# Optimization experiments

Hardware: AMD Instinct MI355X
Metric: run time of the kernel (lower is better)

## Reference

```python
import jax, jax.numpy as jnp
import numpy as np

B, S, T = 128, 1024, 512
VOCAB, E, HE, HD, ATT = 1000, 128, 64, 66, 32


def setup_inputs() -> dict:
    key = jax.random.key(0)
    ks = jax.random.split(key, 14)
    p = lambda k, shape: (jax.random.normal(k, shape, dtype=jnp.float32) * 0.05)
    return {
        'x': jax.random.randint(ks[0], (B, S), 0, VOCAB, dtype=jnp.int32),
        'c': jax.random.normal(ks[1], (B, T), dtype=jnp.float32),
        'emb': p(ks[2], (VOCAB, E)),
        'enc_Wih': p(ks[3], (4 * HE, E)),
        'enc_Whh': p(ks[4], (4 * HE, HE)),
        'enc_b': p(ks[5], (4 * HE,)),
        'att_fc_W': p(ks[6], (HE, E)),
        'att_fc_b': p(ks[7], (HE,)),
        'att_w_W': p(ks[8], (ATT, HE)),
        'att_w_b': p(ks[9], (ATT,)),
        'dec_Wih': p(ks[10], (4 * HD, ATT)),
        'dec_Whh': p(ks[11], (4 * HD, HD)),
        'dec_b': p(ks[12], (4 * HD,)),
        'fin_W': p(ks[13], (E, HD)),
        'fin_b': jnp.zeros((E,), dtype=jnp.float32),
    }


def _lstm_seq(xs, W_ih, W_hh, b, H):
    # xs: [B, S, in]; PyTorch gate order i, f, g, o
    bsz = xs.shape[0]
    gx = jnp.einsum('bsi,gi->bsg', xs, W_ih) + b  # [B,S,4H]

    def step(carry, g_t):
        h, c = carry
        g = g_t + h @ W_hh.T
        i, f, gg, o = jnp.split(g, 4, axis=-1)
        c = jax.nn.sigmoid(f) * c + jax.nn.sigmoid(i) * jnp.tanh(gg)
        h = jax.nn.sigmoid(o) * jnp.tanh(c)
        return (h, c), h

    h0 = jnp.zeros((bsz, H), xs.dtype)
    (_, _), hs = jax.lax.scan(step, (h0, h0), jnp.swapaxes(gx, 0, 1))
    return jnp.swapaxes(hs, 0, 1)  # [B,S,H]


def reference(x, c, emb, enc_Wih, enc_Whh, enc_b, att_fc_W, att_fc_b,
              att_w_W, att_w_b, dec_Wih, dec_Whh, dec_b, fin_W, fin_b):
    # encoder: embed + LSTM, returns full sequence of hidden states [B,S,64]
    enc = _lstm_seq(emb[x], enc_Wih, enc_Whh, enc_b, HE)
    bsz, steps = x.shape[0], c.shape[1]
    # initial decoder input: embedding of token 0, broadcast over batch
    x0 = jnp.broadcast_to(emb[0], (bsz, E))
    h0 = jnp.zeros((bsz, HD), enc.dtype)

    def step(carry, _):
        xemb, h, cc = carry
        # attend(a=xemb, A=enc)
        a = xemb @ att_fc_W.T + att_fc_b                     # [B,64]
        A = a[:, None, :] * enc                              # [B,S,64]
        alpha = jax.nn.softmax(
            jnp.tanh(jnp.einsum('bse,ae->bsa', A, att_w_W) + att_w_b),
            axis=-1)                                         # [B,S,32]
        beta = alpha.sum(axis=1)                             # [B,32]
        # decoder LSTM cell (one timestep)
        g = beta @ dec_Wih.T + h @ dec_Whh.T + dec_b
        i, f, gg, o = jnp.split(g, 4, axis=-1)
        cc = jax.nn.sigmoid(f) * cc + jax.nn.sigmoid(i) * jnp.tanh(gg)
        h = jax.nn.sigmoid(o) * jnp.tanh(cc)
        xemb = h @ fin_W.T + fin_b                           # feed back via final_fc
        return (xemb, h, cc), h

    _, hs = jax.lax.scan(step, (x0, h0, h0), None, length=steps)
    return jnp.swapaxes(hs, 0, 1)  # [B,T,66]
```

## Files before the change

### kernel.cpp

```cpp
#include <hip/hip_runtime.h>
#include <hip/hip_bf16.h>

#define kB 128
#define kS 1024
#define kT 512
#define kV 1000
#define kE 128
#define kHE 64
#define kHD 66
#define kATT 32
#define kGE 256
#define kGD 264

typedef __attribute__((ext_vector_type(4))) float f32x4;
typedef __attribute__((ext_vector_type(8))) short bf16x8;
typedef __attribute__((ext_vector_type(8))) unsigned short u16x8;

__device__ __forceinline__ unsigned short f2bf(float f) {
  unsigned int u = __builtin_bit_cast(unsigned int, f);
  u += 0x7FFFu + ((u >> 16) & 1u);
  return (unsigned short)(u >> 16);
}
__device__ __forceinline__ float rcp_(float x) { return __builtin_amdgcn_rcpf(x); }
__device__ __forceinline__ float fsig(float x)  { return rcp_(1.0f + __expf(-x)); }
__device__ __forceinline__ float ftanh(float x) { return 1.0f - 2.0f * rcp_(1.0f + __expf(2.0f * x)); }
__device__ __forceinline__ float fexp2(float z) {
#if __has_builtin(__builtin_amdgcn_exp2f)
  return __builtin_amdgcn_exp2f(z);
#else
  return __expf(z * 0.6931471805599453f);
#endif
}
__device__ __forceinline__ const unsigned short* launder_us(const unsigned short* p) {
  asm volatile("" : "+s"(p));
  return p;
}
__device__ __forceinline__ float dpp_red16(float v) {
  int x = __builtin_bit_cast(int, v);
  v += __builtin_bit_cast(float, __builtin_amdgcn_update_dpp(0, x, 0xB1, 0xf, 0xf, true));
  x = __builtin_bit_cast(int, v);
  v += __builtin_bit_cast(float, __builtin_amdgcn_update_dpp(0, x, 0x4E, 0xf, 0xf, true));
  x = __builtin_bit_cast(int, v);
  v += __builtin_bit_cast(float, __builtin_amdgcn_update_dpp(0, x, 0x124, 0xf, 0xf, true));
  x = __builtin_bit_cast(int, v);
  v += __builtin_bit_cast(float, __builtin_amdgcn_update_dpp(0, x, 0x128, 0xf, 0xf, true));
  return v;
}
#define DPPB(v, ctrl) __builtin_bit_cast(float, __builtin_amdgcn_update_dpp(0, __builtin_bit_cast(int, (v)), (ctrl), 0xf, 0xf, true))

__global__ __launch_bounds__(256) void prep_kernel(
    const float* __restrict__ emb, const float* __restrict__ enc_Wih,
    const float* __restrict__ enc_b, const float* __restrict__ enc_Whh,
    const float* __restrict__ att_fc_W, const float* __restrict__ att_fc_b,
    const float* __restrict__ att_w_W,
    const float* __restrict__ fin_W, const float* __restrict__ fin_b,
    const float* __restrict__ dec_Wih, const float* __restrict__ dec_Whh,
    const float* __restrict__ dec_b,
    float* __restrict__ embW, unsigned short* __restrict__ decF,
    unsigned short* __restrict__ encF, unsigned short* __restrict__ afF,
    float* __restrict__ wregF, float* __restrict__ dbias,
    float* __restrict__ wh64, float* __restrict__ wh65,
    float* __restrict__ abias, float* __restrict__ ainit) {
  int bid = blockIdx.x, tid = threadIdx.x;
  if (bid < kV) {
    float acc = enc_b[tid];
    const float* er = emb + bid * kE;
    const float* wr = enc_Wih + tid * kE;
    for (int e = 0; e < kE; ++e) acc += er[e] * wr[e];
    embW[bid * kGE + tid] = acc;
  } else if (bid == kV) {
    for (int i = tid; i < 17 * 3 * 64 * 8; i += 256) {
      int jj = i & 7, lane = (i >> 3) & 63, ts = i >> 9;
      int tile = ts / 3, ks = ts - tile * 3;
      int jp = tile * 16 + (lane & 15);
      int cell = jp >> 2, gate = jp & 3;
      int k = ks * 32 + ((lane >> 4) << 3) + jj;
      float v = 0.f;
      if (cell < kHD) {
        int j = gate * kHD + cell;
        if (k < 32) v = dec_Wih[j * kATT + k];
        else v = dec_Whh[j * kHD + (k - 32)];
      }
      decF[i] = f2bf(v);
    }
  } else if (bid == kV + 1) {
    for (int i = tid; i < 16 * 2 * 64 * 8; i += 256) {
      int jj = i & 7, lane = (i >> 3) & 63, ts = i >> 9;
      int tile = ts >> 1, ks = ts & 1;
      int j = tile * 16 + (lane & 15);
      int k = ks * 32 + ((lane >> 4) << 3) + jj;
      encF[i] = f2bf(enc_Whh[j * kHE + k]);
    }
  } else if (bid == kV + 2) {
    for (int i = tid; i < 4 * 3 * 64 * 8; i += 256) {
      int jj = i & 7, lane = (i >> 3) & 63, ts = i >> 9;
      int tile = ts / 3, ks = ts - tile * 3;
      int aidx = tile * 16 + (lane & 15);
      int m = ks * 32 + ((lane >> 4) << 3) + jj;
      float v = 0.f;
      if (m < kHD)
        for (int e = 0; e < kE; ++e) v += att_fc_W[aidx * kE + e] * fin_W[e * kHD + m];
      afF[i] = f2bf(v);
    }
  } else if (bid == kV + 3) {
    for (int i = tid; i < 8 * 64 * 4; i += 256) {
      int c = i & 3, lane = (i >> 2) & 63, jq = i >> 8;
      int half = jq & 1, kc = (jq >> 1) & 1, mt = jq >> 2;
      wregF[i] = att_w_W[(mt * 16 + (lane & 15)) * kHE + kc * 32 + ((lane >> 4) << 3) + half * 4 + c];
    }
  } else if (bid == kV + 4) {
    for (int jp = tid; jp < kGD; jp += 256) {
      int cell = jp >> 2, gate = jp & 3;
      int j = gate * kHD + cell;
      float s = 0.f;
      for (int m = 0; m < kATT; ++m) s += dec_Wih[j * kATT + m];
      dbias[jp] = dec_b[j] + 32.0f * s;
      wh64[jp] = dec_Whh[j * kHD + 64];
      wh65[jp] = dec_Whh[j * kHD + 65];
    }
  } else {
    if (tid < kHE) {
      float acc = att_fc_b[tid];
      for (int e = 0; e < kE; ++e) acc += att_fc_W[tid * kE + e] * fin_b[e];
      abias[tid] = acc;
    } else if (tid < 2 * kHE) {
      int a = tid - kHE;
      float acc = att_fc_b[a];
      for (int e = 0; e < kE; ++e) acc += emb[e] * att_fc_W[a * kE + e];
      ainit[a] = acc;
    }
  }
}

__global__ __launch_bounds__(256)
__attribute__((amdgpu_waves_per_eu(1, 1)))
void enc_kernel(
    const int* __restrict__ x, const float* __restrict__ embW,
    const unsigned short* __restrict__ encF, float* __restrict__ out) {
  __shared__ struct __align__(16) {
    unsigned short xe[64];
    float gbuf[kGE];
    int toks[kS];
  } sm;
  const int b = blockIdx.x, t = threadIdx.x, lane = t & 63, wv = t >> 6;

  for (int i = t; i < kS; i += 256) sm.toks[i] = x[b * kS + i];
  if (t < 64) sm.xe[t] = 0;

  u16x8 eQ[4][2];
  #pragma unroll
  for (int q = 0; q < 4; ++q)
    #pragma unroll
    for (int ks = 0; ks < 2; ++ks)
      eQ[q][ks] = *(const u16x8*)&encF[(((wv * 4 + q) * 2 + ks) * 64 + lane) * 8];
  __syncthreads();

  float gx0 = 0, gx1 = 0, gx2 = 0, gx3 = 0;
  if (lane < 16) {
    int tok = sm.toks[0];
    gx0 = embW[tok * kGE + wv * 64 + 0 + lane];
    gx1 = embW[tok * kGE + wv * 64 + 16 + lane];
    gx2 = embW[tok * kGE + wv * 64 + 32 + lane];
    gx3 = embW[tok * kGE + wv * 64 + 48 + lane];
  }
  float cE = 0.0f;
  unsigned short* eg = (unsigned short*)(out + (size_t)b * (kT * kHD));

  for (int s = 0; s < kS; ++s) {
    union { u16x8 u; bf16x8 v; } xa0, xa1;
    xa0.u = *(const u16x8*)&sm.xe[(lane >> 4) << 3];
    xa1.u = *(const u16x8*)&sm.xe[32 + ((lane >> 4) << 3)];
    float gn0 = 0, gn1 = 0, gn2 = 0, gn3 = 0;
    int tokn = sm.toks[(s + 1 < kS) ? (s + 1) : s];
    if (lane < 16) {
      gn0 = embW[tokn * kGE + wv * 64 + 0 + lane];
      gn1 = embW[tokn * kGE + wv * 64 + 16 + lane];
      gn2 = embW[tokn * kGE + wv * 64 + 32 + lane];
      gn3 = embW[tokn * kGE + wv * 64 + 48 + lane];
    }
    f32x4 z = {0.f, 0.f, 0.f, 0.f};
    f32x4 a0 = __builtin_amdgcn_mfma_f32_16x16x32_bf16(xa0.v, eQ[0][0], z, 0, 0, 0);
    a0 = __builtin_amdgcn_mfma_f32_16x16x32_bf16(xa1.v, eQ[0][1], a0, 0, 0, 0);
    f32x4 a1 = __builtin_amdgcn_mfma_f32_16x16x32_bf16(xa0.v, eQ[1][0], z, 0, 0, 0);
    a1 = __builtin_amdgcn_mfma_f32_16x16x32_bf16(xa1.v, eQ[1][1], a1, 0, 0, 0);
    f32x4 a2 = __builtin_amdgcn_mfma_f32_16x16x32_bf16(xa0.v, eQ[2][0], z, 0, 0, 0);
    a2 = __builtin_amdgcn_mfma_f32_16x16x32_bf16(xa1.v, eQ[2][1], a2, 0, 0, 0);
    f32x4 a3 = __builtin_amdgcn_mfma_f32_16x16x32_bf16(xa0.v, eQ[3][0], z, 0, 0, 0);
    a3 = __builtin_amdgcn_mfma_f32_16x16x32_bf16(xa1.v, eQ[3][1], a3, 0, 0, 0);
    if (lane < 16) {
      sm.gbuf[wv * 64 + 0 + lane]  = a0[0] + gx0;
      sm.gbuf[wv * 64 + 16 + lane] = a1[0] + gx1;
      sm.gbuf[wv * 64 + 32 + lane] = a2[0] + gx2;
      sm.gbuf[wv * 64 + 48 + lane] = a3[0] + gx3;
    }
    __syncthreads();
    if (t < 64) {
      float gi = sm.gbuf[t], gf = sm.gbuf[64 + t], gg = sm.gbuf[128 + t], go = sm.gbuf[192 + t];
      cE = fsig(gf) * cE + fsig(gi) * ftanh(gg);
      float h = fsig(go) * ftanh(cE);
      unsigned short hb = f2bf(h);
      sm.xe[t] = hb;
      eg[s * 64 + ((((t >> 3) ^ (s & 7)) << 3) | (t & 7))] = hb;
    }
    __syncthreads();
    gx0 = gn0; gx1 = gn1; gx2 = gn2; gx3 = gn3;
  }
}

struct __align__(16) DSm {
  unsigned short enc[kS * kHE];
  float wregL[8 * 64 * 4];
  unsigned short afL[4 * 3 * 64 * 8];
  float dbL[kGD];
  float wh64L[kGD];
  float wh65L[kGD];
  float absL[64];
  float aa[64];
  float beta[32];
  unsigned short xv[2][160];
  float hh2[2][2];
};

union U8 { u16x8 u; bf16x8 v; };

__global__ __launch_bounds__(512, 2)
void dec_kernel(
    const float* __restrict__ att_w_b,
    const unsigned short* __restrict__ decF, const unsigned short* __restrict__ afF,
    const float* __restrict__ wregF_ws, const float* __restrict__ dbias_ws,
    const float* __restrict__ wh64_ws, const float* __restrict__ wh65_ws,
    const float* __restrict__ abias_ws, const float* __restrict__ ainit_ws,
    float* __restrict__ out) {
  __shared__ DSm sm;
  const int b = blockIdx.x, t = threadIdx.x, lane = t & 63, wv = t >> 6;
  const int lr = lane & 15, g = lane >> 4;

  {
    const u16x8* src = (const u16x8*)(out + (size_t)b * (kT * kHD));
    u16x8* dst = (u16x8*)sm.enc;
    #pragma unroll
    for (int i = 0; i < 16; ++i) dst[t + i * 512] = src[t + i * 512];
  }
  ((f32x4*)sm.wregL)[t] = ((const f32x4*)wregF_ws)[t];
  for (int i = t; i < 768; i += 512) ((u16x8*)sm.afL)[i] = ((const u16x8*)afF)[i];
  for (int i = t; i < kGD; i += 512) {
    sm.dbL[i] = dbias_ws[i];
    sm.wh64L[i] = wh64_ws[i];
    sm.wh65L[i] = wh65_ws[i];
  }
  if (t < 64) { sm.absL[t] = abias_ws[t]; sm.aa[t] = ainit_ws[t]; }
  if (t < 32) sm.beta[t] = 0.f;
  for (int i = t; i < 320; i += 512) ((unsigned short*)sm.xv)[i] = 0;
  if (t < 4) ((float*)sm.hh2)[t] = 0.f;

  f32x4 wb0, wb1;
  #pragma unroll
  for (int r = 0; r < 4; ++r) {
    wb0[r] = att_w_b[g * 4 + r];
    wb1[r] = att_w_b[16 + g * 4 + r];
  }
  const int sbase = wv * 128;
  const int tileA = wv, tileB = wv + 8;
  const bool has3 = (wv == 7);

  U8 qa[3], qb[3];
  #pragma unroll
  for (int ks = 0; ks < 3; ++ks) {
    qa[ks].u = *(const u16x8*)&decF[((tileA * 3 + ks) * 64 + lane) * 8];
    qb[ks].u = *(const u16x8*)&decF[((tileB * 3 + ks) * 64 + lane) * 8];
  }
  float cDa = 0.0f, cDb = 0.0f, cDc = 0.0f;
  __syncthreads();

  for (int step = 0; step < kT; ++step) {
    const int cb = step & 1, nb = cb ^ 1;
    U8 qc[3];
    {
      const f32x4* aap = (const f32x4*)sm.aa;
      const f32x4* wrl = (const f32x4*)sm.wregL;
      bf16x8 af[2][2];
      #pragma unroll
      for (int kc = 0; kc < 2; ++kc) {
        f32x4 a0v = aap[kc * 8 + g * 2];
        f32x4 a1v = aap[kc * 8 + g * 2 + 1];
        #pragma unroll
        for (int mt = 0; mt < 2; ++mt) {
          f32x4 w0 = wrl[((mt * 2 + kc) * 2 + 0) * 64 + lane];
          f32x4 w1 = wrl[((mt * 2 + kc) * 2 + 1) * 64 + lane];
          union { bf16x8 v; __hip_bfloat162 h2[4]; } tmp;
          tmp.h2[0] = __float22bfloat162_rn(make_float2(w0.x * a0v.x, w0.y * a0v.y));
          tmp.h2[1] = __float22bfloat162_rn(make_float2(w0.z * a0v.z, w0.w * a0v.w));
          tmp.h2[2] = __float22bfloat162_rn(make_float2(w1.x * a1v.x, w1.y * a1v.y));
          tmp.h2[3] = __float22bfloat162_rn(make_float2(w1.z * a1v.z, w1.w * a1v.w));
          af[mt][kc] = tmp.v;
        }
      }
      float betaAcc[2][4] = {};
      float amax = 0.0f;
      #pragma unroll
      for (int nt = 0; nt < 8; ++nt) {
        int s = sbase + nt * 16 + lr;
        int sw = s & 7;
        U8 e0, e1;
        e0.u = *(const u16x8*)&sm.enc[s * kHE + ((g ^ sw) << 3)];
        e1.u = *(const u16x8*)&sm.enc[s * kHE + (((4 + g) ^ sw) << 3)];
        f32x4 acc0 = __builtin_amdgcn_mfma_f32_16x16x32_bf16(af[0][0], e0.v, wb0, 0, 0, 0);
        acc0 = __builtin_amdgcn_mfma_f32_16x16x32_bf16(af[0][1], e1.v, acc0, 0, 0, 0);
        f32x4 acc1 = __builtin_amdgcn_mfma_f32_16x16x32_bf16(af[1][0], e0.v, wb1, 0, 0, 0);
        acc1 = __builtin_amdgcn_mfma_f32_16x16x32_bf16(af[1][1], e1.v, acc1, 0, 0, 0);
        float u0[4], u1[4], dsum = 0.f;
        #pragma unroll
        for (int r = 0; r < 4; ++r) {
          float x0 = acc0[r], x1 = acc1[r];
          amax = fmaxf(amax, fmaxf(__builtin_fabsf(x0), __builtin_fabsf(x1)));
          u0[r] = fexp2(x0 * __builtin_fmaf(x0 * x0, -0.48089835f, 1.44269504f));
          u1[r] = fexp2(x1 * __builtin_fmaf(x1 * x1, -0.48089835f, 1.44269504f));
          dsum += u0[r] + u1[r];
        }
        dsum += __shfl_xor(dsum, 16);
        dsum += __shfl_xor(dsum, 32);
        float invd = rcp_(dsum);
        #pragma unroll
        for (int r = 0; r < 4; ++r) {
          betaAcc[0][r] += u0[r] * invd;
          betaAcc[1][r] += u1[r] * invd;
        }
      }
      if (__builtin_expect(__any(amax > 0.35f), 0)) {
        #pragma unroll
        for (int mt = 0; mt < 2; ++mt)
          #pragma unroll
          for (int r = 0; r < 4; ++r) betaAcc[mt][r] = 0.f;
        for (int nt = 0; nt < 8; ++nt) {
          int s = sbase + nt * 16 + lr;
          int sw = s & 7;
          U8 e0, e1;
          e0.u = *(const u16x8*)&sm.enc[s * kHE + ((g ^ sw) << 3)];
          e1.u = *(const u16x8*)&sm.enc[s * kHE + (((4 + g) ^ sw) << 3)];
          f32x4 acc0 = __builtin_amdgcn_mfma_f32_16x16x32_bf16(af[0][0], e0.v, wb0, 0, 0, 0);
          acc0 = __builtin_amdgcn_mfma_f32_16x16x32_bf16(af[0][1], e1.v, acc0, 0, 0, 0);
          f32x4 acc1 = __builtin_amdgcn_mfma_f32_16x16x32_bf16(af[1][0], e0.v, wb1, 0, 0, 0);
          acc1 = __builtin_amdgcn_mfma_f32_16x16x32_bf16(af[1][1], e1.v, acc1, 0, 0, 0);
          float u0[4], u1[4], dsum = 0.f;
          for (int r = 0; r < 4; ++r) {
            u0[r] = __expf(tanhf(acc0[r]));
            u1[r] = __expf(tanhf(acc1[r]));
            dsum += u0[r] + u1[r];
          }
          dsum += __shfl_xor(dsum, 16);
          dsum += __shfl_xor(dsum, 32);
          float invd = rcp_(dsum);
          for (int r = 0; r < 4; ++r) {
            betaAcc[0][r] += u0[r] * invd;
            betaAcc[1][r] += u1[r] * invd;
          }
        }
      }
      if (has3) {
        const unsigned short* dFp = launder_us(decF);
        #pragma unroll
        for (int ks = 0; ks < 3; ++ks)
          qc[ks].u = *(const u16x8*)&dFp[((16 * 3 + ks) * 64 + lane) * 8];
      }
      #pragma unroll
      for (int mt = 0; mt < 2; ++mt)
        #pragma unroll
        for (int r = 0; r < 4; ++r) {
          float v = dpp_red16(betaAcc[mt][r]);
          if (lr == 0) atomicAdd(&sm.beta[mt * 16 + g * 4 + r], v);
        }
    }
    __syncthreads();
    {
      const f32x4* pb = (const f32x4*)sm.beta;
      f32x4 b0 = pb[g * 2], b1 = pb[g * 2 + 1];
      union { bf16x8 v; __hip_bfloat162 h2[4]; } bfr;
      bfr.h2[0] = __float22bfloat162_rn(make_float2(b0.x - 32.f, b0.y - 32.f));
      bfr.h2[1] = __float22bfloat162_rn(make_float2(b0.z - 32.f, b0.w - 32.f));
      bfr.h2[2] = __float22bfloat162_rn(make_float2(b1.x - 32.f, b1.y - 32.f));
      bfr.h2[3] = __float22bfloat162_rn(make_float2(b1.z - 32.f, b1.w - 32.f));
      U8 xg1, xg2;
      xg1.u = *(const u16x8*)&sm.xv[cb][32 + (g << 3)];
      xg2.u = *(const u16x8*)&sm.xv[cb][64 + (g << 3)];
      float hh0 = sm.hh2[cb][0], hh1 = sm.hh2[cb][1];
      float* op = out + ((size_t)b * kT + step) * kHD;
      const int gate = lane & 3;
      const float kk = (gate == 2) ? 2.0f : 1.0f;
      f32x4 z = {0.f, 0.f, 0.f, 0.f};
      {
        f32x4 ga = __builtin_amdgcn_mfma_f32_16x16x32_bf16(bfr.v, qa[0].v, z, 0, 0, 0);
        ga = __builtin_amdgcn_mfma_f32_16x16x32_bf16(xg1.v, qa[1].v, ga, 0, 0, 0);
        ga = __builtin_amdgcn_mfma_f32_16x16x32_bf16(xg2.v, qa[2].v, ga, 0, 0, 0);
        int jp = tileA * 16 + lr;
        float xg = ga[0] + sm.dbL[jp] + sm.wh64L[jp] * hh0 + sm.wh65L[jp] * hh1;
        float y = fsig(kk * xg);
        float v = (gate == 2) ? (2.0f * y - 1.0f) : y;
        float q0 = DPPB(v, 0x00), q1 = DPPB(v, 0x55), q2 = DPPB(v, 0xAA), q3 = DPPB(v, 0xFF);
        float cn = q1 * cDa + q0 * q2;
        cDa = cn;
        float h = q3 * ftanh(cn);
        if (gate == 0 && lane < 16) {
          int cell = jp >> 2;
          sm.xv[nb][32 + cell] = f2bf(h);
          op[cell] = h;
        }
      }
      {
        f32x4 gb = __builtin_amdgcn_mfma_f32_16x16x32_bf16(bfr.v, qb[0].v, z, 0, 0, 0);
        gb = __builtin_amdgcn_mfma_f32_16x16x32_bf16(xg1.v, qb[1].v, gb, 0, 0, 0);
        gb = __builtin_amdgcn_mfma_f32_16x16x32_bf16(xg2.v, qb[2].v, gb, 0, 0, 0);
        int jp = tileB * 16 + lr;
        float xg = gb[0] + sm.dbL[jp] + sm.wh64L[jp] * hh0 + sm.wh65L[jp] * hh1;
        float y = fsig(kk * xg);
        float v = (gate == 2) ? (2.0f * y - 1.0f) : y;
        float q0 = DPPB(v, 0x00), q1 = DPPB(v, 0x55), q2 = DPPB(v, 0xAA), q3 = DPPB(v, 0xFF);
        float cn = q1 * cDb + q0 * q2;
        cDb = cn;
        float h = q3 * ftanh(cn);
        if (gate == 0 && lane < 16) {
          int cell = jp >> 2;
          sm.xv[nb][32 + cell] = f2bf(h);
          op[cell] = h;
        }
      }
      if (has3) {
        f32x4 gc = __builtin_amdgcn_mfma_f32_16x16x32_bf16(bfr.v, qc[0].v, z, 0, 0, 0);
        gc = __builtin_amdgcn_mfma_f32_16x16x32_bf16(xg1.v, qc[1].v, gc, 0, 0, 0);
        gc = __builtin_amdgcn_mfma_f32_16x16x32_bf16(xg2.v, qc[2].v, gc, 0, 0, 0);
        int jp = 256 + (lane & 7);
        float xg = gc[0] + sm.dbL[jp] + sm.wh64L[jp] * hh0 + sm.wh65L[jp] * hh1;
        float y = fsig(kk * xg);
        float v = (gate == 2) ? (2.0f * y - 1.0f) : y;
        float q0 = DPPB(v, 0x00), q1 = DPPB(v, 0x55), q2 = DPPB(v, 0xAA), q3 = DPPB(v, 0xFF);
        float cn = q1 * cDc + q0 * q2;
        cDc = cn;
        float h = q3 * ftanh(cn);
        if (gate == 0 && lane < 8) {
          int cell = 64 + (lane >> 2);
          sm.xv[nb][32 + cell] = f2bf(h);
          sm.hh2[nb][lane >> 2] = h;
          op[cell] = h;
        }
      }
    }
    __syncthreads();
    if (wv == 0) {
      U8 y0, y1, y2;
      y0.u = *(const u16x8*)&sm.xv[nb][32 + (g << 3)];
      y1.u = *(const u16x8*)&sm.xv[nb][64 + (g << 3)];
      y2.u = *(const u16x8*)&sm.xv[nb][96 + (g << 3)];
      f32x4 z = {0.f, 0.f, 0.f, 0.f};
      #pragma unroll
      for (int tt = 0; tt < 4; ++tt) {
        U8 f0, f1, f2;
        f0.u = *(const u16x8*)&sm.afL[((tt * 3 + 0) * 64 + lane) * 8];
        f1.u = *(const u16x8*)&sm.afL[((tt * 3 + 1) * 64 + lane) * 8];
        f2.u = *(const u16x8*)&sm.afL[((tt * 3 + 2) * 64 + lane) * 8];
        f32x4 acc = __builtin_amdgcn_mfma_f32_16x16x32_bf16(y0.v, f0.v, z, 0, 0, 0);
        acc = __builtin_amdgcn_mfma_f32_16x16x32_bf16(y1.v, f1.v, acc, 0, 0, 0);
        acc = __builtin_amdgcn_mfma_f32_16x16x32_bf16(y2.v, f2.v, acc, 0, 0, 0);
        if (lane < 16) sm.aa[tt * 16 + lane] = acc[0] + sm.absL[tt * 16 + lane];
      }
      if (lane < 32) sm.beta[lane] = 0.f;
    }
    __syncthreads();
  }
}

extern "C" void kernel_launch(void* const* d_in, const int* in_sizes, int n_in,
                              void* d_out, int out_size, void* d_ws, size_t ws_size,
                              hipStream_t stream) {
  const int*   x        = (const int*)d_in[0];
  const float* emb      = (const float*)d_in[2];
  const float* enc_Wih  = (const float*)d_in[3];
  const float* enc_Whh  = (const float*)d_in[4];
  const float* enc_b    = (const float*)d_in[5];
  const float* att_fc_W = (const float*)d_in[6];
  const float* att_fc_b = (const float*)d_in[7];
  const float* att_w_W  = (const float*)d_in[8];
  const float* att_w_b  = (const float*)d_in[9];
  const float* dec_Wih  = (const float*)d_in[10];
  const float* dec_Whh  = (const float*)d_in[11];
  const float* dec_b    = (const float*)d_in[12];
  const float* fin_W    = (const float*)d_in[13];
  const float* fin_b    = (const float*)d_in[14];
  float* out = (float*)d_out;

  float* embW = (float*)d_ws;
  unsigned short* decF = (unsigned short*)(embW + kV * kGE);
  unsigned short* encF = decF + 17 * 3 * 64 * 8;
  unsigned short* afF  = encF + 16 * 2 * 64 * 8;
  float* wregF = (float*)(afF + 4 * 3 * 64 * 8);
  float* dbias = wregF + 8 * 64 * 4;
  float* wh64  = dbias + kGD;
  float* wh65  = wh64 + kGD;
  float* abias = wh65 + kGD;
  float* ainit = abias + kHE;

  prep_kernel<<<dim3(kV + 6), dim3(256), 0, stream>>>(
      emb, enc_Wih, enc_b, enc_Whh, att_fc_W, att_fc_b, att_w_W, fin_W, fin_b,
      dec_Wih, dec_Whh, dec_b, embW, decF, encF, afF, wregF, dbias, wh64, wh65,
      abias, ainit);
  enc_kernel<<<dim3(kB), dim3(256), 0, stream>>>(x, embW, encF, out);
  dec_kernel<<<dim3(kB), dim3(512), 0, stream>>>(
      att_w_b, decF, afF, wregF, dbias, wh64, wh65, abias, ainit, out);
}
```

Before: 2.823 ms.

## Interleave encoder LSTM gates per cell and fuse cell update into MFMA waves

Reorders the encoder gate weights and the precomputed embedding-gate table so the four gates of each cell sit in adjacent lanes. Each wave then computes the cell update in registers with DPP broadcasts, and tanh is expressed through a scaled sigmoid. The hidden-state buffer is double-buffered, which removes the shared gate buffer and one of the two barriers per timestep on the serial critical path. The cost is redundant activation math across lanes and reliance on the DPPB macro for lane shuffles.

```diff
diff --git a/kernel.cpp b/kernel.cpp
--- a/kernel.cpp
+++ b/kernel.cpp
@@ -67,7 +67,7 @@
     const float* er = emb + bid * kE;
     const float* wr = enc_Wih + tid * kE;
     for (int e = 0; e < kE; ++e) acc += er[e] * wr[e];
-    embW[bid * kGE + tid] = acc;
+    embW[bid * kGE + (tid & 63) * 4 + (tid >> 6)] = acc;
   } else if (bid == kV) {
     for (int i = tid; i < 17 * 3 * 64 * 8; i += 256) {
       int jj = i & 7, lane = (i >> 3) & 63, ts = i >> 9;
@@ -87,7 +87,9 @@
     for (int i = tid; i < 16 * 2 * 64 * 8; i += 256) {
       int jj = i & 7, lane = (i >> 3) & 63, ts = i >> 9;
       int tile = ts >> 1, ks = ts & 1;
-      int j = tile * 16 + (lane & 15);
+      int jp = tile * 16 + (lane & 15);
+      int cell = jp >> 2, gate = jp & 3;
+      int j = gate * kHE + cell;
       int k = ks * 32 + ((lane >> 4) << 3) + jj;
       encF[i] = f2bf(enc_Whh[j * kHE + k]);
     }
@@ -138,14 +140,16 @@
     const int* __restrict__ x, const float* __restrict__ embW,
     const unsigned short* __restrict__ encF, float* __restrict__ out) {
   __shared__ struct __align__(16) {
-    unsigned short xe[64];
-    float gbuf[kGE];
+    unsigned short xe[2][64];
     int toks[kS];
   } sm;
   const int b = blockIdx.x, t = threadIdx.x, lane = t & 63, wv = t >> 6;
+  const int lr = lane & 15;
+  const int gate = lane & 3;
+  const float kk = (gate == 2) ? 2.0f : 1.0f;
 
   for (int i = t; i < kS; i += 256) sm.toks[i] = x[b * kS + i];
-  if (t < 64) sm.xe[t] = 0;
+  if (t < 128) ((unsigned short*)sm.xe)[t] = 0;
 
   u16x8 eQ[4][2];
   #pragma unroll
@@ -155,55 +159,47 @@
       eQ[q][ks] = *(const u16x8*)&encF[(((wv * 4 + q) * 2 + ks) * 64 + lane) * 8];
   __syncthreads();
 
-  float gx0 = 0, gx1 = 0, gx2 = 0, gx3 = 0;
-  if (lane < 16) {
+  float gxq[4];
+  {
     int tok = sm.toks[0];
-    gx0 = embW[tok * kGE + wv * 64 + 0 + lane];
-    gx1 = embW[tok * kGE + wv * 64 + 16 + lane];
-    gx2 = embW[tok * kGE + wv * 64 + 32 + lane];
-    gx3 = embW[tok * kGE + wv * 64 + 48 + lane];
-  }
-  float cE = 0.0f;
+    #pragma unroll
+    for (int q = 0; q < 4; ++q) gxq[q] = embW[tok * kGE + wv * 64 + q * 16 + lr];
+  }
+  float cEq[4] = {0.f, 0.f, 0.f, 0.f};
   unsigned short* eg = (unsigned short*)(out + (size_t)b * (kT * kHD));
 
   for (int s = 0; s < kS; ++s) {
+    const int cb = s & 1, nb = cb ^ 1;
     union { u16x8 u; bf16x8 v; } xa0, xa1;
-    xa0.u = *(const u16x8*)&sm.xe[(lane >> 4) << 3];
-    xa1.u = *(const u16x8*)&sm.xe[32 + ((lane >> 4) << 3)];
-    float gn0 = 0, gn1 = 0, gn2 = 0, gn3 = 0;
+    xa0.u = *(const u16x8*)&sm.xe[cb][(lane >> 4) << 3];
+    xa1.u = *(const u16x8*)&sm.xe[cb][32 + ((lane >> 4) << 3)];
+    float gn[4];
     int tokn = sm.toks[(s + 1 < kS) ? (s + 1) : s];
-    if (lane < 16) {
-      gn0 = embW[tokn * kGE + wv * 64 + 0 + lane];
-      gn1 = embW[tokn * kGE + wv * 64 + 16 + lane];
-      gn2 = embW[tokn * kGE + wv * 64 + 32 + lane];
-      gn3 = embW[tokn * kGE + wv * 64 + 48 + lane];
-    }
+    #pragma unroll
+    for (int q = 0; q < 4; ++q) gn[q] = embW[tokn * kGE + wv * 64 + q * 16 + lr];
+
     f32x4 z = {0.f, 0.f, 0.f, 0.f};
-    f32x4 a0 = __builtin_amdgcn_mfma_f32_16x16x32_bf16(xa0.v, eQ[0][0], z, 0, 0, 0);
-    a0 = __builtin_amdgcn_mfma_f32_16x16x32_bf16(xa1.v, eQ[0][1], a0, 0, 0, 0);
-    f32x4 a1 = __builtin_amdgcn_mfma_f32_16x16x32_bf16(xa0.v, eQ[1][0], z, 0, 0, 0);
-    a1 = __builtin_amdgcn_mfma_f32_16x16x32_bf16(xa1.v, eQ[1][1], a1, 0, 0, 0);
-    f32x4 a2 = __builtin_amdgcn_mfma_f32_16x16x32_bf16(xa0.v, eQ[2][0], z, 0, 0, 0);
-    a2 = __builtin_amdgcn_mfma_f32_16x16x32_bf16(xa1.v, eQ[2][1], a2, 0, 0, 0);
-    f32x4 a3 = __builtin_amdgcn_mfma_f32_16x16x32_bf16(xa0.v, eQ[3][0], z, 0, 0, 0);
-    a3 = __builtin_amdgcn_mfma_f32_16x16x32_bf16(xa1.v, eQ[3][1], a3, 0, 0, 0);
-    if (lane < 16) {
-      sm.gbuf[wv * 64 + 0 + lane]  = a0[0] + gx0;
-      sm.gbuf[wv * 64 + 16 + lane] = a1[0] + gx1;
-      sm.gbuf[wv * 64 + 32 + lane] = a2[0] + gx2;
-      sm.gbuf[wv * 64 + 48 + lane] = a3[0] + gx3;
-    }
+    #pragma unroll
+    for (int q = 0; q < 4; ++q) {
+      f32x4 a = __builtin_amdgcn_mfma_f32_16x16x32_bf16(xa0.v, eQ[q][0], z, 0, 0, 0);
+      a = __builtin_amdgcn_mfma_f32_16x16x32_bf16(xa1.v, eQ[q][1], a, 0, 0, 0);
+      float xg = a[0] + gxq[q];
+      float y = fsig(kk * xg);
+      float v = (gate == 2) ? (2.0f * y - 1.0f) : y;
+      float q0 = DPPB(v, 0x00), q1 = DPPB(v, 0x55), q2 = DPPB(v, 0xAA), q3 = DPPB(v, 0xFF);
+      float cn = q1 * cEq[q] + q0 * q2;
+      cEq[q] = cn;
+      float h = q3 * ftanh(cn);
+      if (gate == 0 && lane < 16) {
+        int cell = (wv * 4 + q) * 4 + (lr >> 2);
+        unsigned short hb = f2bf(h);
+        sm.xe[nb][cell] = hb;
+        eg[s * 64 + ((((cell >> 3) ^ (s & 7)) << 3) | (cell & 7))] = hb;
+      }
+    }
+    #pragma unroll
+    for (int q = 0; q < 4; ++q) gxq[q] = gn[q];
     __syncthreads();
-    if (t < 64) {
-      float gi = sm.gbuf[t], gf = sm.gbuf[64 + t], gg = sm.gbuf[128 + t], go = sm.gbuf[192 + t];
-      cE = fsig(gf) * cE + fsig(gi) * ftanh(gg);
-      float h = fsig(go) * ftanh(cE);
-      unsigned short hb = f2bf(h);
-      sm.xe[t] = hb;
-      eg[s * 64 + ((((t >> 3) ^ (s & 7)) << 3) | (t & 7))] = hb;
-    }
-    __syncthreads();
-    gx0 = gn0; gx1 = gn1; gx2 = gn2; gx3 = gn3;
   }
 }
 
```

Result: slower. 2.944 ms (+4.3%).
